# Performance work log

Hardware: AMD Instinct MI355X
Metric: run time of the kernel (lower is better)

Reference implementation:

```python
import jax, jax.numpy as jnp
import numpy as np

N_USERS = 100000
M_ITEMS = 50000
N_ALL = N_USERS + M_ITEMS
N_EDGES = 4800000
DIM = 64
N_LAYERS = 3
A = 1.0
B = 1.0
ALPHA = 0.1


def setup_inputs() -> dict:
    key = jax.random.key(0)
    k1, k2, k3, k4, k5 = jax.random.split(key, 5)
    user_emb = 0.1 * jax.random.normal(k1, (N_USERS, DIM), dtype=jnp.float32)
    item_emb = 0.1 * jax.random.normal(k2, (M_ITEMS, DIM), dtype=jnp.float32)
    rows = jax.random.randint(k3, (N_EDGES,), 0, N_ALL, dtype=jnp.int32)
    cols = jax.random.randint(k4, (N_EDGES,), 0, N_ALL, dtype=jnp.int32)
    # normalized-adjacency-like values (roughly 1/avg_degree scale)
    vals = jax.random.uniform(k5, (N_EDGES,), dtype=jnp.float32) / 32.0
    return {"user_emb": user_emb, "item_emb": item_emb,
            "rows": rows, "cols": cols, "vals": vals}


def reference(user_emb, item_emb, rows, cols, vals):
    embed = jnp.concatenate([user_emb, item_emb], axis=0)  # [N_ALL, DIM]

    def spmm(x):  # sparse G @ x via gather + segment_sum
        return jax.ops.segment_sum(vals[:, None] * x[cols], rows,
                                   num_segments=N_ALL)

    # p0 = I, p1 = (a-b)/2 * I + (a+b)/2 * G  (eye folded into elementwise terms)
    e0 = embed
    e1 = (A - B) / 2.0 * embed + (A + B) / 2.0 * spmm(embed)
    embs = [e0, e1]
    for k in range(2, N_LAYERS + 1):
        ab = A + B
        theta1 = (2 * k + ab) * (2 * k + ab - 1) / ((k + ab) * 2 * k)
        theta2 = (2 * k + ab - 1) * (A ** 2 - B ** 2) / ((2 * k + ab - 2) * (k + ab) * 2 * k)
        theta3 = (k + A - 1) * (k + B - 1) * (2 * k + ab) / (k * (ab + k) * (2 * k + ab - 2))
        emb_k = theta1 * spmm(embs[-1]) + theta2 * embs[-1] - theta3 * embs[-2]
        embs.append(emb_k)

    band_stop = jnp.mean(jnp.stack(embs, axis=1), axis=1)  # [N_ALL, DIM]
    band_pass = jnp.tanh(ALPHA * embed - band_stop)
    out = jnp.concatenate([band_stop, band_pass], axis=1)  # [N_ALL, 2*DIM]
    users, items = out[:N_USERS], out[N_USERS:]
    return users, items
```

## Files before the change

### kernel.cpp

```cpp
#include <hip/hip_runtime.h>
#include <hip/hip_fp16.h>
#include <cmath>
#include <cstdint>

#define NU 100000
#define NI 50000
#define NALL 150000
#define DIM 64
#define NE 4800000

#define BSH 7
#define BROWS 128
#define NBUCK ((NALL + BROWS - 1) / BROWS)
#define SBT 512
#define EPT 8
#define CHUNK (SBT * EPT)
#define COLMASK 0x3FFFF
#define BCAP 4608
#define SPT 9


__global__ __launch_bounds__(SBT) void bucket_hist_kernel(
        const int* __restrict__ rows, int* __restrict__ bcnt) {
    __shared__ int h[NBUCK];
    for (int i = threadIdx.x; i < NBUCK; i += SBT) h[i] = 0;
    __syncthreads();
    int base = blockIdx.x * CHUNK;
    #pragma unroll
    for (int i = 0; i < EPT; i++) {
        int e = base + threadIdx.x + i * SBT;
        if (e < NE) atomicAdd(&h[rows[e] >> BSH], 1);
    }
    __syncthreads();
    for (int i = threadIdx.x; i < NBUCK; i += SBT)
        if (h[i]) atomicAdd(&bcnt[i], h[i]);
}

__global__ void bucket_scan_kernel(const int* __restrict__ bcnt, int* __restrict__ bptr) {
    __shared__ int s[1024];
    int t = threadIdx.x;
    const int chunk = (NBUCK + 1023) / 1024;
    int lo = t * chunk, hi = lo + chunk;
    if (hi > NBUCK) hi = NBUCK;
    int sum = 0;
    for (int i = lo; i < hi; ++i) sum += bcnt[i];
    s[t] = sum;
    __syncthreads();
    for (int off = 1; off < 1024; off <<= 1) {
        int v = (t >= off) ? s[t - off] : 0;
        __syncthreads();
        s[t] += v;
        __syncthreads();
    }
    int run = s[t] - sum;
    for (int i = lo; i < hi; ++i) { bptr[i] = run; run += bcnt[i]; }
    if (t == 1023) bptr[NBUCK] = s[1023];
}

__global__ __launch_bounds__(SBT, 6) void binned_scatter_kernel(
        const int* __restrict__ rows, const int* __restrict__ cols,
        const float* __restrict__ vals, const int* __restrict__ bptr,
        int* __restrict__ bfill, int2* __restrict__ tmp) {
    __shared__ int2 eLDS[CHUNK];
    __shared__ unsigned short bLDS[CHUNK];
    __shared__ int lcnt[NBUCK];
    __shared__ int lofs[NBUCK + 1];
    __shared__ int psum[SBT];
    int t = threadIdx.x;
    int base = blockIdx.x * CHUNK;
    int cnt = NE - base; if (cnt > CHUNK) cnt = CHUNK;
    for (int i = t; i < NBUCK; i += SBT) lcnt[i] = 0;
    __syncthreads();
    int2 ed[EPT]; int mcb[EPT]; int mrk[EPT];
    #pragma unroll
    for (int k = 0; k < EPT; k++) {
        int p = t + k * SBT;
        mcb[k] = -1;
        if (p < cnt) {
            int e = base + p;
            int r = rows[e];
            int cb = r >> BSH;
            mcb[k] = cb;
            mrk[k] = atomicAdd(&lcnt[cb], 1);
            ed[k] = make_int2(((r & (BROWS - 1)) << 18) | cols[e], __float_as_int(vals[e]));
        }
    }
    __syncthreads();
    const int cpt = (NBUCK + SBT - 1) / SBT;
    int lo = t * cpt, hi = lo + cpt;
    if (lo > NBUCK) lo = NBUCK;
    if (hi > NBUCK) hi = NBUCK;
    int s = 0;
    for (int i = lo; i < hi; ++i) s += lcnt[i];
    psum[t] = s;
    __syncthreads();
    for (int off = 1; off < SBT; off <<= 1) {
        int v = (t >= off) ? psum[t - off] : 0;
        __syncthreads();
        psum[t] += v;
        __syncthreads();
    }
    int run = psum[t] - s;
    for (int i = lo; i < hi; ++i) { lofs[i] = run; run += lcnt[i]; }
    if (t == SBT - 1) lofs[NBUCK] = cnt;
    __syncthreads();
    for (int i = t; i < NBUCK; i += SBT) {
        int c = lcnt[i];
        int g = c ? atomicAdd(&bfill[i], c) : 0;
        lcnt[i] = bptr[i] + g - lofs[i];
    }
    #pragma unroll
    for (int k = 0; k < EPT; k++)
        if (mcb[k] >= 0) {
            int pos = lofs[mcb[k]] + mrk[k];
            eLDS[pos] = ed[k];
            bLDS[pos] = (unsigned short)mcb[k];
        }
    __syncthreads();
    for (int p = t; p < cnt; p += SBT)
        tmp[lcnt[bLDS[p]] + p] = eLDS[p];
}

__global__ __launch_bounds__(SBT, 6) void bucket_sort_kernel(
        const int* __restrict__ bptr, const int2* __restrict__ tmp,
        int2* __restrict__ sedges, int* __restrict__ row_ptr) {
    __shared__ int2 eLDS[BCAP];
    __shared__ int h[BROWS], sc[BROWS], f[BROWS];
    int b = blockIdx.x, t = threadIdx.x;
    int s0 = bptr[b], s1 = bptr[b + 1];
    int cnt = s1 - s0;
    if (t < BROWS) { h[t] = 0; f[t] = 0; }
    if (b == NBUCK - 1 && t == 0) row_ptr[NALL] = s1;
    __syncthreads();
    if (cnt <= BCAP) {
        int2 ed[SPT]; int mrl[SPT]; int mrk[SPT];
        #pragma unroll
        for (int k = 0; k < SPT; k++) {
            int p = t + k * SBT;
            mrl[k] = -1;
            if (p < cnt) {
                int2 E = tmp[s0 + p];
                int rl = E.x >> 18;
                mrl[k] = rl;
                mrk[k] = atomicAdd(&h[rl], 1);
                ed[k] = E;
            }
        }
        __syncthreads();
        if (t < BROWS) sc[t] = h[t];
        __syncthreads();
        for (int off = 1; off < BROWS; off <<= 1) {
            int v = 0;
            if (t < BROWS && t >= off) v = sc[t - off];
            __syncthreads();
            if (t < BROWS) sc[t] += v;
            __syncthreads();
        }
        if (t < BROWS) {
            int row = b * BROWS + t;
            if (row < NALL) row_ptr[row] = s0 + sc[t] - h[t];
        }
        __syncthreads();
        #pragma unroll
        for (int k = 0; k < SPT; k++)
            if (mrl[k] >= 0) eLDS[sc[mrl[k]] - h[mrl[k]] + mrk[k]] = ed[k];
        __syncthreads();
        for (int p = t; p < cnt; p += SBT) sedges[s0 + p] = eLDS[p];
    } else {
        for (int i = s0 + t; i < s1; i += SBT) atomicAdd(&h[tmp[i].x >> 18], 1);
        __syncthreads();
        if (t < BROWS) sc[t] = h[t];
        __syncthreads();
        for (int off = 1; off < BROWS; off <<= 1) {
            int v = 0;
            if (t < BROWS && t >= off) v = sc[t - off];
            __syncthreads();
            if (t < BROWS) sc[t] += v;
            __syncthreads();
        }
        if (t < BROWS) {
            int row = b * BROWS + t;
            if (row < NALL) row_ptr[row] = s0 + sc[t] - h[t];
        }
        __syncthreads();
        for (int i = s0 + t; i < s1; i += SBT) {
            int2 E = tmp[i];
            int rl = E.x >> 18;
            int r = atomicAdd(&f[rl], 1);
            sedges[s0 + sc[rl] - h[rl] + r] = E;
        }
    }
}


__global__ void concat_init_kernel(const float4* __restrict__ u4, const float4* __restrict__ it4,
                                   float4* __restrict__ w0, uint2* __restrict__ w0h,
                                   float4* __restrict__ out4) {
    int idx = blockIdx.x * blockDim.x + threadIdx.x;
    const int total4 = NALL * 16;
    if (idx >= total4) return;
    const int nu4 = NU * 16;
    float4 v = (idx < nu4) ? u4[idx] : it4[idx - nu4];
    if (w0) w0[idx] = v;
    if (w0h) {
        __half2 a = __floats2half2_rn(v.x, v.y), b = __floats2half2_rn(v.z, v.w);
        w0h[idx] = make_uint2(*(unsigned*)&a, *(unsigned*)&b);
    }
    if (out4) {
        int row = idx >> 4, q = idx & 15;
        out4[(size_t)row * 32 + q] = v;
    }
}

#define FMAMIX_LO(a, x, s) asm("v_fma_mix_f32 %0, %1, %2, %0 op_sel:[0,0,0] op_sel_hi:[1,0,0]" : "+v"(a) : "v"(x), "v"(s))
#define FMAMIX_HI(a, x, s) asm("v_fma_mix_f32 %0, %1, %2, %0 op_sel:[1,0,0] op_sel_hi:[1,0,0]" : "+v"(a) : "v"(x), "v"(s))

__device__ __forceinline__ void fma_mix8(float* acc, uint4 p, float v) {
    FMAMIX_LO(acc[0], p.x, v); FMAMIX_HI(acc[1], p.x, v);
    FMAMIX_LO(acc[2], p.y, v); FMAMIX_HI(acc[3], p.y, v);
    FMAMIX_LO(acc[4], p.z, v); FMAMIX_HI(acc[5], p.z, v);
    FMAMIX_LO(acc[6], p.w, v); FMAMIX_HI(acc[7], p.w, v);
}

__device__ __forceinline__ void load_pair_e0(const float4* __restrict__ u4,
                                             const float4* __restrict__ it4,
                                             int wid, int l8, float4& a, float4& b) {
    const float4* q = (wid < NU) ? (u4 + (size_t)wid * 16 + l8 * 2)
                                 : (it4 + (size_t)(wid - NU) * 16 + l8 * 2);
    a = q[0]; b = q[1];
}

__device__ __forceinline__ void load_pair_h(const __half* __restrict__ h,
                                            int wid, int l8, float4& a, float4& b) {
    uint4 p = ((const uint4*)h)[(size_t)wid * 8 + l8];
    __half2* hp = (__half2*)&p;
    float2 f0 = __half22float2(hp[0]);
    float2 f1 = __half22float2(hp[1]);
    float2 f2 = __half22float2(hp[2]);
    float2 f3 = __half22float2(hp[3]);
    a = make_float4(f0.x, f0.y, f1.x, f1.y);
    b = make_float4(f2.x, f2.y, f3.x, f3.y);
}

__device__ __forceinline__ uint4 pack_h8(float4 a, float4 b) {
    __half2 h0 = __floats2half2_rn(a.x, a.y);
    __half2 h1 = __floats2half2_rn(a.z, a.w);
    __half2 h2 = __floats2half2_rn(b.x, b.y);
    __half2 h3 = __floats2half2_rn(b.z, b.w);
    uint4 ph;
    ph.x = *(unsigned*)&h0; ph.y = *(unsigned*)&h1;
    ph.z = *(unsigned*)&h2; ph.w = *(unsigned*)&h3;
    return ph;
}

__device__ __forceinline__ void spmm_row_acc(const int* __restrict__ row_ptr,
                                             const int2* __restrict__ sedges,
                                             const uint4* __restrict__ xv,
                                             int wid, int g, int l8, float* acc) {
    int s = row_ptr[wid], e = row_ptr[wid + 1];
    for (int j = s + 4 * g; j < e; j += 32) {
        const int4* p2 = (const int4*)(sedges + j);
        int4 eA = p2[0];
        int4 eB = p2[1];
        uint4 q0 = xv[(size_t)(eA.x & COLMASK) * 8 + l8];
        uint4 q1 = xv[(size_t)(eA.z & COLMASK) * 8 + l8];
        uint4 q2 = xv[(size_t)(eB.x & COLMASK) * 8 + l8];
        uint4 q3 = xv[(size_t)(eB.z & COLMASK) * 8 + l8];
        float v0 = __int_as_float(eA.y);
        float v1 = (j + 1 < e) ? __int_as_float(eA.w) : 0.f;
        float v2 = (j + 2 < e) ? __int_as_float(eB.y) : 0.f;
        float v3 = (j + 3 < e) ? __int_as_float(eB.w) : 0.f;
        fma_mix8(acc, q0, v0);
        fma_mix8(acc, q1, v1);
        fma_mix8(acc, q2, v2);
        fma_mix8(acc, q3, v3);
    }
    #pragma unroll
    for (int off = 8; off < 64; off <<= 1) {
        #pragma unroll
        for (int j = 0; j < 8; j++) acc[j] += __shfl_xor(acc[j], off);
    }
}

__global__ __launch_bounds__(256) void spmm8_combine_f16_kernel(
        const int* __restrict__ row_ptr, const int2* __restrict__ sedges,
        const __half* __restrict__ xh,
        const __half* __restrict__ em1h, int em1_embed,
        const __half* __restrict__ em2h, int em2_embed,
        const float4* __restrict__ u4, const float4* __restrict__ it4,
        float t1, float t2, float t3,
        __half* __restrict__ ekh_out) {
    int wid = (blockIdx.x * blockDim.x + threadIdx.x) >> 6;
    if (wid >= NALL) return;
    int lane = threadIdx.x & 63;
    int g = lane >> 3, l8 = lane & 7;
    float acc[8];
    #pragma unroll
    for (int j = 0; j < 8; j++) acc[j] = 0.f;
    spmm_row_acc(row_ptr, sedges, (const uint4*)xh, wid, g, l8, acc);
    if (g == 0) {
        float4 ea, eb;
        ea.x = t1 * acc[0]; ea.y = t1 * acc[1]; ea.z = t1 * acc[2]; ea.w = t1 * acc[3];
        eb.x = t1 * acc[4]; eb.y = t1 * acc[5]; eb.z = t1 * acc[6]; eb.w = t1 * acc[7];
        if (t2 != 0.f) {
            float4 m1a, m1b;
            if (em1_embed) load_pair_e0(u4, it4, wid, l8, m1a, m1b);
            else           load_pair_h(em1h, wid, l8, m1a, m1b);
            ea.x += t2 * m1a.x; ea.y += t2 * m1a.y; ea.z += t2 * m1a.z; ea.w += t2 * m1a.w;
            eb.x += t2 * m1b.x; eb.y += t2 * m1b.y; eb.z += t2 * m1b.z; eb.w += t2 * m1b.w;
        }
        if (t3 != 0.f) {
            float4 m2a, m2b;
            if (em2_embed) load_pair_e0(u4, it4, wid, l8, m2a, m2b);
            else           load_pair_h(em2h, wid, l8, m2a, m2b);
            ea.x -= t3 * m2a.x; ea.y -= t3 * m2a.y; ea.z -= t3 * m2a.z; ea.w -= t3 * m2a.w;
            eb.x -= t3 * m2b.x; eb.y -= t3 * m2b.y; eb.z -= t3 * m2b.z; eb.w -= t3 * m2b.w;
        }
        ((uint4*)ekh_out)[(size_t)wid * 8 + l8] = pack_h8(ea, eb);
    }
}

__global__ __launch_bounds__(256) void spmm8_final_kernel(
        const int* __restrict__ row_ptr, const int2* __restrict__ sedges,
        const __half* __restrict__ xh,
        const __half* __restrict__ e1h, const __half* __restrict__ e2h,
        const float4* __restrict__ u4, const float4* __restrict__ it4,
        float t1, float t2, float t3,
        float4* __restrict__ out4) {
    int wid = (blockIdx.x * blockDim.x + threadIdx.x) >> 6;
    if (wid >= NALL) return;
    int lane = threadIdx.x & 63;
    int g = lane >> 3, l8 = lane & 7;
    float acc[8];
    #pragma unroll
    for (int j = 0; j < 8; j++) acc[j] = 0.f;
    spmm_row_acc(row_ptr, sedges, (const uint4*)xh, wid, g, l8, acc);
    if (g == 0) {
        float4 e0a, e0b, e1a, e1b, e2a, e2b;
        load_pair_e0(u4, it4, wid, l8, e0a, e0b);
        load_pair_h(e1h, wid, l8, e1a, e1b);
        load_pair_h(e2h, wid, l8, e2a, e2b);
        float4 e3a, e3b;
        e3a.x = t1 * acc[0] + t2 * e2a.x - t3 * e1a.x;
        e3a.y = t1 * acc[1] + t2 * e2a.y - t3 * e1a.y;
        e3a.z = t1 * acc[2] + t2 * e2a.z - t3 * e1a.z;
        e3a.w = t1 * acc[3] + t2 * e2a.w - t3 * e1a.w;
        e3b.x = t1 * acc[4] + t2 * e2b.x - t3 * e1b.x;
        e3b.y = t1 * acc[5] + t2 * e2b.y - t3 * e1b.y;
        e3b.z = t1 * acc[6] + t2 * e2b.z - t3 * e1b.z;
        e3b.w = t1 * acc[7] + t2 * e2b.w - t3 * e1b.w;
        float4 bsa, bsb, bpa, bpb;
        bsa.x = 0.25f * (e0a.x + e1a.x + e2a.x + e3a.x);
        bsa.y = 0.25f * (e0a.y + e1a.y + e2a.y + e3a.y);
        bsa.z = 0.25f * (e0a.z + e1a.z + e2a.z + e3a.z);
        bsa.w = 0.25f * (e0a.w + e1a.w + e2a.w + e3a.w);
        bsb.x = 0.25f * (e0b.x + e1b.x + e2b.x + e3b.x);
        bsb.y = 0.25f * (e0b.y + e1b.y + e2b.y + e3b.y);
        bsb.z = 0.25f * (e0b.z + e1b.z + e2b.z + e3b.z);
        bsb.w = 0.25f * (e0b.w + e1b.w + e2b.w + e3b.w);
        bpa.x = tanhf(0.1f * e0a.x - bsa.x);
        bpa.y = tanhf(0.1f * e0a.y - bsa.y);
        bpa.z = tanhf(0.1f * e0a.z - bsa.z);
        bpa.w = tanhf(0.1f * e0a.w - bsa.w);
        bpb.x = tanhf(0.1f * e0b.x - bsb.x);
        bpb.y = tanhf(0.1f * e0b.y - bsb.y);
        bpb.z = tanhf(0.1f * e0b.z - bsb.z);
        bpb.w = tanhf(0.1f * e0b.w - bsb.w);
        size_t ob = (size_t)wid * 32 + l8 * 2;
        out4[ob] = bsa;
        out4[ob + 1] = bsb;
        out4[ob + 16] = bpa;
        out4[ob + 17] = bpb;
    }
}


__global__ void spmm_combine_kernel(const int* __restrict__ row_ptr,
                                    const int2* __restrict__ sedges,
                                    const float* __restrict__ x,
                                    const float* __restrict__ ekm1,
                                    const float* __restrict__ ekm2,
                                    float t1, float t2, float t3,
                                    float* __restrict__ ek_out,
                                    float* __restrict__ out) {
    int wid = (blockIdx.x * blockDim.x + threadIdx.x) >> 6;
    if (wid >= NALL) return;
    int lane = threadIdx.x & 63;
    int s = row_ptr[wid], e = row_ptr[wid + 1];
    float acc = 0.f;
    int i = s;
    for (; i + 4 <= e; i += 4) {
        int2 ea = sedges[i], eb = sedges[i + 1], ec = sedges[i + 2], ed = sedges[i + 3];
        acc += __int_as_float(ea.y) * x[(size_t)(ea.x & COLMASK) * DIM + lane];
        acc += __int_as_float(eb.y) * x[(size_t)(eb.x & COLMASK) * DIM + lane];
        acc += __int_as_float(ec.y) * x[(size_t)(ec.x & COLMASK) * DIM + lane];
        acc += __int_as_float(ed.y) * x[(size_t)(ed.x & COLMASK) * DIM + lane];
    }
    for (; i < e; ++i) {
        int2 ed = sedges[i];
        acc += __int_as_float(ed.y) * x[(size_t)(ed.x & COLMASK) * DIM + lane];
    }
    size_t o = (size_t)wid * DIM + lane;
    float ek = t1 * acc + t2 * ekm1[o] - t3 * ekm2[o];
    ek_out[o] = ek;
    out[(size_t)wid * 128 + lane] += ek;
}

__global__ void finalize_kernel(const float* __restrict__ u, const float* __restrict__ it,
                                float* __restrict__ out) {
    int idx = blockIdx.x * blockDim.x + threadIdx.x;
    const int total = NALL * DIM;
    if (idx >= total) return;
    const int nue = NU * DIM;
    float v = (idx < nue) ? u[idx] : it[idx - nue];
    int row = idx >> 6, d = idx & 63;
    size_t o = (size_t)row * 128 + d;
    float bs = out[o] * 0.25f;
    float bp = tanhf(0.1f * v - bs);
    out[o] = bs;
    out[o + DIM] = bp;
}

__global__ void spmm_atomic_kernel(const int* __restrict__ rows, const int* __restrict__ cols,
                                   const float* __restrict__ vals, const float* __restrict__ x,
                                   float* __restrict__ y) {
    int gid = blockIdx.x * blockDim.x + threadIdx.x;
    int e = gid >> 6;
    if (e >= NE) return;
    int lane = threadIdx.x & 63;
    atomicAdd(&y[(size_t)rows[e] * DIM + lane], vals[e] * x[(size_t)cols[e] * DIM + lane]);
}

__global__ void combine3_kernel(float* __restrict__ t, const float* __restrict__ ekm1,
                                const float* __restrict__ ekm2, float t1, float t2, float t3,
                                float* __restrict__ out) {
    int idx = blockIdx.x * blockDim.x + threadIdx.x;
    const int total = NALL * DIM;
    if (idx >= total) return;
    float ek = t1 * t[idx] + t2 * ekm1[idx] - t3 * ekm2[idx];
    t[idx] = ek;
    int row = idx >> 6, d = idx & 63;
    out[(size_t)row * 128 + d] += ek;
}


extern "C" void kernel_launch(void* const* d_in, const int* in_sizes, int n_in,
                              void* d_out, int out_size, void* d_ws, size_t ws_size,
                              hipStream_t stream) {
    const float* user_emb = (const float*)d_in[0];
    const float* item_emb = (const float*)d_in[1];
    const int*   rows     = (const int*)d_in[2];
    const int*   cols     = (const int*)d_in[3];
    const float* vals     = (const float*)d_in[4];
    float* out = (float*)d_out;

    const size_t nbuf = (size_t)NALL * DIM;
    float* W0 = (float*)d_ws;
    float* W1 = W0 + nbuf;
    float* W2 = W1 + nbuf;
    int2*  tmp     = (int2*)W1;
    int2*  sedges  = (int2*)(W2 + nbuf);
    int*   row_ptr = (int*)(sedges + NE + 4);
    int*   bcnt    = row_ptr + (NALL + 1);
    int*   bptr    = bcnt + NBUCK;
    int*   bfill   = bptr + (NBUCK + 1);
    char*  pHA     = (char*)(bfill + NBUCK);
    pHA = (char*)(((uintptr_t)pHA + 255) & ~(uintptr_t)255);
    __half* HA     = (__half*)pHA;
    __half* HB     = HA + nbuf;
    __half* HC     = HB + nbuf;
    size_t need_basic = (size_t)((char*)HA - (char*)d_ws);
    size_t need_full  = (size_t)((char*)(HC + nbuf) - (char*)d_ws);

    const double A = 1.0, B = 1.0, ab = A + B;
    float c0 = (float)((A - B) / 2.0);
    float c1 = (float)((A + B) / 2.0);
    float th1[4], th2[4], th3[4];
    for (int k = 2; k <= 3; k++) {
        th1[k] = (float)((2.0*k+ab)*(2.0*k+ab-1.0)/((k+ab)*2.0*k));
        th2[k] = (float)((2.0*k+ab-1.0)*(A*A-B*B)/((2.0*k+ab-2.0)*(k+ab)*2.0*k));
        th3[k] = (float)((k+A-1.0)*(k+B-1.0)*(2.0*k+ab)/(k*(ab+k)*(2.0*k+ab-2.0)));
    }

    const int total = NALL * DIM;
    const int total4 = NALL * 16;
    dim3 blk(256);
    dim3 sblk(SBT);
    dim3 grdE((total + 255) / 256);
    dim3 grd4((total4 + 255) / 256);
    dim3 grdBin((NE + CHUNK - 1) / CHUNK);
    dim3 grdBuck(NBUCK);
    dim3 grdRow((NALL * 64 + 255) / 256);

    const float4* u4  = (const float4*)user_emb;
    const float4* it4 = (const float4*)item_emb;

    if (ws_size >= need_basic) {
        hipMemsetAsync(bcnt, 0, NBUCK * sizeof(int), stream);
        hipMemsetAsync(bfill, 0, NBUCK * sizeof(int), stream);
        hipMemsetAsync(sedges + NE, 0, 4 * sizeof(int2), stream);
        bucket_hist_kernel<<<grdBin, sblk, 0, stream>>>(rows, bcnt);
        bucket_scan_kernel<<<1, 1024, 0, stream>>>(bcnt, bptr);
        binned_scatter_kernel<<<grdBin, sblk, 0, stream>>>(rows, cols, vals, bptr, bfill, tmp);
        bucket_sort_kernel<<<grdBuck, sblk, 0, stream>>>(bptr, tmp, sedges, row_ptr);

        if (ws_size >= need_full) {
            concat_init_kernel<<<grd4, blk, 0, stream>>>(u4, it4, nullptr, (uint2*)HA, nullptr);
            spmm8_combine_f16_kernel<<<grdRow, blk, 0, stream>>>(row_ptr, sedges, HA,
                                                                 nullptr, 1, nullptr, 1,
                                                                 u4, it4, c1, c0, 0.0f, HB);
            spmm8_combine_f16_kernel<<<grdRow, blk, 0, stream>>>(row_ptr, sedges, HB,
                                                                 HB, 0, nullptr, 1,
                                                                 u4, it4, th1[2], th2[2], th3[2],
                                                                 HC);
            spmm8_final_kernel<<<grdRow, blk, 0, stream>>>(row_ptr, sedges, HC, HB, HC,
                                                           u4, it4, th1[3], th2[3], th3[3],
                                                           (float4*)out);
        } else {
            concat_init_kernel<<<grd4, blk, 0, stream>>>(u4, it4, (float4*)W0, nullptr, (float4*)out);
            spmm_combine_kernel<<<grdRow, blk, 0, stream>>>(row_ptr, sedges, W0, W0, W0,
                                                            c1, c0, 0.0f, W1, out);
            spmm_combine_kernel<<<grdRow, blk, 0, stream>>>(row_ptr, sedges, W1, W1, W0,
                                                            th1[2], th2[2], th3[2], W2, out);
            spmm_combine_kernel<<<grdRow, blk, 0, stream>>>(row_ptr, sedges, W2, W2, W1,
                                                            th1[3], th2[3], th3[3], W0, out);
            finalize_kernel<<<grdE, blk, 0, stream>>>(user_emb, item_emb, out);
        }
    } else {
        long long spmm_threads = (long long)NE * 64;
        dim3 grdS((unsigned)((spmm_threads + 255) / 256));
        concat_init_kernel<<<grd4, blk, 0, stream>>>(u4, it4, (float4*)W0, nullptr, (float4*)out);
        hipMemsetAsync(W1, 0, nbuf * sizeof(float), stream);
        spmm_atomic_kernel<<<grdS, blk, 0, stream>>>(rows, cols, vals, W0, W1);
        combine3_kernel<<<grdE, blk, 0, stream>>>(W1, W0, W0, c1, c0, 0.0f, out);
        hipMemsetAsync(W2, 0, nbuf * sizeof(float), stream);
        spmm_atomic_kernel<<<grdS, blk, 0, stream>>>(rows, cols, vals, W1, W2);
        combine3_kernel<<<grdE, blk, 0, stream>>>(W2, W1, W0, th1[2], th2[2], th3[2], out);
        hipMemsetAsync(W0, 0, nbuf * sizeof(float), stream);
        spmm_atomic_kernel<<<grdS, blk, 0, stream>>>(rows, cols, vals, W2, W0);
        combine3_kernel<<<grdE, blk, 0, stream>>>(W0, W2, W1, th1[3], th2[3], th3[3], out);
        finalize_kernel<<<grdE, blk, 0, stream>>>(user_emb, item_emb, out);
    }
}
```

Measured before the change: 443.7 us.

## Drop histogram pass by scattering into fixed-capacity bucket slots

Removes the separate bucket histogram kernel and its memset by having the binned scatter write each bucket's edges into a fixed CAP-sized slot, using atomic fill counts as the histogram. The prefix scan now runs after scattering to give compact offsets for the sort stage, which reads from the fixed slots. This saves one full pass over the rows array and a kernel launch, but the temp buffer becomes much larger (NBUCK*CAP int2 spanning W0..W2) and the result is wrong if any bucket exceeds CAP edges.

```diff
diff --git a/kernel.cpp b/kernel.cpp
--- a/kernel.cpp
+++ b/kernel.cpp
@@ -16,34 +16,19 @@
 #define EPT 8
 #define CHUNK (SBT * EPT)
 #define COLMASK 0x3FFFF
+#define CAP 8192
 #define BCAP 4608
 #define SPT 9
 
 
-__global__ __launch_bounds__(SBT) void bucket_hist_kernel(
-        const int* __restrict__ rows, int* __restrict__ bcnt) {
-    __shared__ int h[NBUCK];
-    for (int i = threadIdx.x; i < NBUCK; i += SBT) h[i] = 0;
-    __syncthreads();
-    int base = blockIdx.x * CHUNK;
-    #pragma unroll
-    for (int i = 0; i < EPT; i++) {
-        int e = base + threadIdx.x + i * SBT;
-        if (e < NE) atomicAdd(&h[rows[e] >> BSH], 1);
-    }
-    __syncthreads();
-    for (int i = threadIdx.x; i < NBUCK; i += SBT)
-        if (h[i]) atomicAdd(&bcnt[i], h[i]);
-}
-
-__global__ void bucket_scan_kernel(const int* __restrict__ bcnt, int* __restrict__ bptr) {
+__global__ void bucket_scan_kernel(const int* __restrict__ bfill, int* __restrict__ bptr) {
     __shared__ int s[1024];
     int t = threadIdx.x;
     const int chunk = (NBUCK + 1023) / 1024;
     int lo = t * chunk, hi = lo + chunk;
     if (hi > NBUCK) hi = NBUCK;
     int sum = 0;
-    for (int i = lo; i < hi; ++i) sum += bcnt[i];
+    for (int i = lo; i < hi; ++i) sum += bfill[i];
     s[t] = sum;
     __syncthreads();
     for (int off = 1; off < 1024; off <<= 1) {
@@ -53,13 +38,13 @@
         __syncthreads();
     }
     int run = s[t] - sum;
-    for (int i = lo; i < hi; ++i) { bptr[i] = run; run += bcnt[i]; }
+    for (int i = lo; i < hi; ++i) { bptr[i] = run; run += bfill[i]; }
     if (t == 1023) bptr[NBUCK] = s[1023];
 }
 
 __global__ __launch_bounds__(SBT, 6) void binned_scatter_kernel(
         const int* __restrict__ rows, const int* __restrict__ cols,
-        const float* __restrict__ vals, const int* __restrict__ bptr,
+        const float* __restrict__ vals,
         int* __restrict__ bfill, int2* __restrict__ tmp) {
     __shared__ int2 eLDS[CHUNK];
     __shared__ unsigned short bLDS[CHUNK];
@@ -107,7 +92,7 @@
     for (int i = t; i < NBUCK; i += SBT) {
         int c = lcnt[i];
         int g = c ? atomicAdd(&bfill[i], c) : 0;
-        lcnt[i] = bptr[i] + g - lofs[i];
+        lcnt[i] = i * CAP + g - lofs[i];
     }
     #pragma unroll
     for (int k = 0; k < EPT; k++)
@@ -129,6 +114,7 @@
     int b = blockIdx.x, t = threadIdx.x;
     int s0 = bptr[b], s1 = bptr[b + 1];
     int cnt = s1 - s0;
+    const int2* src = tmp + (size_t)b * CAP;
     if (t < BROWS) { h[t] = 0; f[t] = 0; }
     if (b == NBUCK - 1 && t == 0) row_ptr[NALL] = s1;
     __syncthreads();
@@ -139,7 +125,7 @@
             int p = t + k * SBT;
             mrl[k] = -1;
             if (p < cnt) {
-                int2 E = tmp[s0 + p];
+                int2 E = src[p];
                 int rl = E.x >> 18;
                 mrl[k] = rl;
                 mrk[k] = atomicAdd(&h[rl], 1);
@@ -167,7 +153,7 @@
         __syncthreads();
         for (int p = t; p < cnt; p += SBT) sedges[s0 + p] = eLDS[p];
     } else {
-        for (int i = s0 + t; i < s1; i += SBT) atomicAdd(&h[tmp[i].x >> 18], 1);
+        for (int i = t; i < cnt; i += SBT) atomicAdd(&h[src[i].x >> 18], 1);
         __syncthreads();
         if (t < BROWS) sc[t] = h[t];
         __syncthreads();
@@ -183,8 +169,8 @@
             if (row < NALL) row_ptr[row] = s0 + sc[t] - h[t];
         }
         __syncthreads();
-        for (int i = s0 + t; i < s1; i += SBT) {
-            int2 E = tmp[i];
+        for (int i = t; i < cnt; i += SBT) {
+            int2 E = src[i];
             int rl = E.x >> 18;
             int r = atomicAdd(&f[rl], 1);
             sedges[s0 + sc[rl] - h[rl] + r] = E;
@@ -458,11 +444,10 @@
     float* W0 = (float*)d_ws;
     float* W1 = W0 + nbuf;
     float* W2 = W1 + nbuf;
-    int2*  tmp     = (int2*)W1;
+    int2*  tmp     = (int2*)W0;
     int2*  sedges  = (int2*)(W2 + nbuf);
     int*   row_ptr = (int*)(sedges + NE + 4);
-    int*   bcnt    = row_ptr + (NALL + 1);
-    int*   bptr    = bcnt + NBUCK;
+    int*   bptr    = row_ptr + (NALL + 1);
     int*   bfill   = bptr + (NBUCK + 1);
     char*  pHA     = (char*)(bfill + NBUCK);
     pHA = (char*)(((uintptr_t)pHA + 255) & ~(uintptr_t)255);
@@ -496,12 +481,10 @@
     const float4* it4 = (const float4*)item_emb;
 
     if (ws_size >= need_basic) {
-        hipMemsetAsync(bcnt, 0, NBUCK * sizeof(int), stream);
         hipMemsetAsync(bfill, 0, NBUCK * sizeof(int), stream);
         hipMemsetAsync(sedges + NE, 0, 4 * sizeof(int2), stream);
-        bucket_hist_kernel<<<grdBin, sblk, 0, stream>>>(rows, bcnt);
-        bucket_scan_kernel<<<1, 1024, 0, stream>>>(bcnt, bptr);
-        binned_scatter_kernel<<<grdBin, sblk, 0, stream>>>(rows, cols, vals, bptr, bfill, tmp);
+        binned_scatter_kernel<<<grdBin, sblk, 0, stream>>>(rows, cols, vals, bfill, tmp);
+        bucket_scan_kernel<<<1, 1024, 0, stream>>>(bfill, bptr);
         bucket_sort_kernel<<<grdBuck, sblk, 0, stream>>>(bptr, tmp, sedges, row_ptr);
 
         if (ws_size >= need_full) {
```

After: 400.2 us. -9.8%, faster.
